# Kernel tuning notes

Hardware: AMD Instinct MI355X
Metric: run time of the kernel (lower is better)

The kernel has to match this reference:

```python
import jax, jax.numpy as jnp
import numpy as np

N_NODES = 100000
N_EDGES = 3200000
NUM_FEATURES = 5
HIDDEN = 64


def _gcn_layer(x, W, b, src, dst, norm, n_nodes):
    """One GCNConv: out = scatter_add(norm * (xW)[src] -> dst) + b.
    src/dst/norm already include self-loops and symmetric normalization."""
    h = x @ W                                  # [N, out_ch] small dense GEMM
    msg = h[src] * norm[:, None]               # [E+N, out_ch] gather + scale
    out = jax.ops.segment_sum(msg, dst, num_segments=n_nodes)
    return out + b


def _build_norm(edge_index, n_nodes):
    """Add self-loops, compute D^{-1/2}[src] * D^{-1/2}[dst] (GCN symmetric norm)."""
    loop = jnp.arange(n_nodes, dtype=edge_index.dtype)
    src = jnp.concatenate([edge_index[0], loop])
    dst = jnp.concatenate([edge_index[1], loop])
    deg = jax.ops.segment_sum(jnp.ones_like(dst, dtype=jnp.float32), dst,
                              num_segments=n_nodes)
    dis = jnp.where(deg > 0, jax.lax.rsqrt(deg), 0.0)  # deg^{-1/2}
    norm = dis[src] * dis[dst]
    return src, dst, norm


def setup_inputs() -> dict:
    key = jax.random.key(0)
    ks = jax.random.split(key, 8)
    x = jax.random.normal(ks[0], (N_NODES, NUM_FEATURES), dtype=jnp.float32)
    edge_index = jax.random.randint(ks[1], (2, N_EDGES), 0, N_NODES, dtype=jnp.int64)
    # glorot-ish scaled params
    W1 = jax.random.normal(ks[2], (NUM_FEATURES, HIDDEN), dtype=jnp.float32) * (1.0 / np.sqrt(NUM_FEATURES))
    b1 = jnp.zeros((HIDDEN,), dtype=jnp.float32)
    W2 = jax.random.normal(ks[3], (HIDDEN, HIDDEN), dtype=jnp.float32) * (1.0 / np.sqrt(HIDDEN))
    b2 = jnp.zeros((HIDDEN,), dtype=jnp.float32)
    W3 = jax.random.normal(ks[4], (HIDDEN, 1), dtype=jnp.float32) * (1.0 / np.sqrt(HIDDEN))
    b3 = jnp.zeros((1,), dtype=jnp.float32)
    return {"x": x, "edge_index": edge_index,
            "W1": W1, "b1": b1, "W2": W2, "b2": b2, "W3": W3, "b3": b3}


def reference(x, edge_index, W1, b1, W2, b2, W3, b3):
    n_nodes = x.shape[0]
    src, dst, norm = _build_norm(edge_index, n_nodes)
    h = jax.nn.relu(_gcn_layer(x, W1, b1, src, dst, norm, n_nodes))
    h = jax.nn.relu(_gcn_layer(h, W2, b2, src, dst, norm, n_nodes))
    out = _gcn_layer(h, W3, b3, src, dst, norm, n_nodes)  # [N, 1]
    return out
```

## Files before the change

kernel.cpp:

```cpp
#include <hip/hip_runtime.h>
#include <hip/hip_fp16.h>

#define NFEAT 5
#define HID 64
#define BSH 8
#define BNODES 256
#define NBK2 512
#define CHUNK 4096
#define ECAPMAX 12288

__global__ void k_binit(int* bcur, int ecap) {
    bcur[threadIdx.x] = threadIdx.x * ecap;
}

__global__ __launch_bounds__(256) void
k_bin(const int* __restrict__ src, const int* __restrict__ dst,
      int* bcur, unsigned* __restrict__ binned, int E) {
    __shared__ unsigned stg[CHUNK];
    __shared__ unsigned short bkt[CHUNK];
    __shared__ int hist[NBK2], base[NBK2], gb[NBK2];
    __shared__ int tmp[256];
    int t = threadIdx.x;
    int e0 = blockIdx.x * CHUNK;
    int cc = E - e0; if (cc > CHUNK) cc = CHUNK;
    hist[t] = 0; hist[t + 256] = 0;
    __syncthreads();
    unsigned me[16]; int mb[16]; unsigned short mr[16];
    const int4* src4 = (const int4*)(src + e0);
    const int4* dst4 = (const int4*)(dst + e0);
#pragma unroll
    for (int k = 0; k < 4; ++k) {
        int i4 = k * 256 + t;
        int ib = i4 * 4;
        int ss[4], dd[4];
        bool any = false;
        if (e0 + ib + 3 < E) {
            int4 s4 = src4[i4], d4 = dst4[i4];
            ss[0]=s4.x; ss[1]=s4.y; ss[2]=s4.z; ss[3]=s4.w;
            dd[0]=d4.x; dd[1]=d4.y; dd[2]=d4.z; dd[3]=d4.w;
            any = true;
#pragma unroll
            for (int j = 0; j < 4; ++j) mb[k*4+j] = 0;
        } else {
#pragma unroll
            for (int j = 0; j < 4; ++j) {
                if (e0 + ib + j < E) { ss[j]=src[e0+ib+j]; dd[j]=dst[e0+ib+j]; any=true; mb[k*4+j]=0; }
                else mb[k*4+j] = -1;
            }
        }
        if (any) {
#pragma unroll
            for (int j = 0; j < 4; ++j) {
                int idx = k * 4 + j;
                if (mb[idx] >= 0) {
                    mb[idx] = dd[j] >> BSH;
                    me[idx] = (unsigned)ss[j] | ((unsigned)(dd[j] & (BNODES - 1)) << 17);
                    mr[idx] = (unsigned short)atomicAdd(&hist[mb[idx]], 1);
                }
            }
        }
    }
    __syncthreads();
    int c0 = hist[2*t], c1 = hist[2*t + 1];
    int s = c0 + c1;
    tmp[t] = s;
    __syncthreads();
    for (int off = 1; off < 256; off <<= 1) {
        int a = (t >= off) ? tmp[t - off] : 0;
        __syncthreads();
        tmp[t] += a;
        __syncthreads();
    }
    int excl = tmp[t] - s;
    base[2*t]     = excl;
    base[2*t + 1] = excl + c0;
    gb[2*t]     = c0 ? atomicAdd(&bcur[2*t], c0) : 0;
    gb[2*t + 1] = c1 ? atomicAdd(&bcur[2*t + 1], c1) : 0;
    __syncthreads();
#pragma unroll
    for (int k = 0; k < 16; ++k)
        if (mb[k] >= 0) {
            int p = base[mb[k]] + mr[k];
            stg[p] = me[k];
            bkt[p] = (unsigned short)mb[k];
        }
    __syncthreads();
#pragma unroll
    for (int k = 0; k < 16; ++k) {
        int p = k * 256 + t;
        if (p < cc) {
            int b = bkt[p];
            binned[gb[b] + (p - base[b])] = stg[p];
        }
    }
}

__global__ __launch_bounds__(256) void
k_sort(const unsigned* __restrict__ binned, const int* __restrict__ bcur,
       const float* __restrict__ x, int* __restrict__ rpN, int* __restrict__ rpE,
       int* __restrict__ csr, float* __restrict__ dis, float* __restrict__ xs,
       int n, int ecap) {
    __shared__ unsigned short rank[ECAPMAX];
    __shared__ int hist[BNODES];
    __shared__ int cur[BNODES];
    __shared__ int tmp[256];
    int t = threadIdx.x, b = blockIdx.x;
    int e0 = b * ecap;
    int cnt = bcur[b] - e0;
    if (cnt > ecap) cnt = ecap;
    int v0 = b << BSH;
    int nv = n - v0; if (nv > BNODES) nv = BNODES;
    hist[t] = 0;
    __syncthreads();
    for (int i = t; i < cnt; i += 256) {
        int vl = binned[e0 + i] >> 17;
        rank[i] = (unsigned short)atomicAdd(&hist[vl], 1);
    }
    __syncthreads();
    if (t < nv) {
        int v = v0 + t;
        float dv = rsqrtf((float)hist[t] + 1.0f);
        dis[v] = dv;
        const float* xr = x + (size_t)v * NFEAT;
        float* xw = xs + (size_t)v * 8;
        xw[0] = dv * xr[0]; xw[1] = dv * xr[1]; xw[2] = dv * xr[2];
        xw[3] = dv * xr[3]; xw[4] = dv * xr[4];
        xw[5] = 0.f; xw[6] = 0.f; xw[7] = 0.f;
    }
    int c = hist[t];
    tmp[t] = c;
    __syncthreads();
    for (int off = 1; off < 256; off <<= 1) {
        int a = (t >= off) ? tmp[t - off] : 0;
        __syncthreads();
        tmp[t] += a;
        __syncthreads();
    }
    int excl = e0 + tmp[t] - c;
    cur[t] = excl;
    if (t < nv) { rpN[v0 + t] = excl; rpE[v0 + t] = excl + c; }
    __syncthreads();
    for (int i = t; i < cnt; i += 256) {
        unsigned e = binned[e0 + i];
        int vl = e >> 17;
        csr[cur[vl] + rank[i]] = (int)(e & 0x1FFFF);
    }
}

__global__ __launch_bounds__(256) void
k_layer1(const int* __restrict__ rpN, const int* __restrict__ rpE,
         const int* __restrict__ csr, const float* __restrict__ xs,
         const float* __restrict__ dis, const float* __restrict__ W1,
         const float* __restrict__ b1, __half* __restrict__ g1h, int n) {
    int wave = (blockIdx.x * blockDim.x + threadIdx.x) >> 6;
    int lane = threadIdx.x & 63;
    if (wave >= n) return;
    int v = wave;
    int r0 = rpN[v], r1 = rpE[v];
    float a0 = 0.f, a1 = 0.f, a2 = 0.f, a3 = 0.f, a4 = 0.f;
    for (int j = r0 + lane; j < r1; j += 64) {
        const float4* q = (const float4*)(xs + (size_t)csr[j] * 8);
        float4 qa = q[0], qb = q[1];
        a0 += qa.x; a1 += qa.y; a2 += qa.z; a3 += qa.w; a4 += qb.x;
    }
#pragma unroll
    for (int m = 32; m > 0; m >>= 1) {
        a0 += __shfl_xor(a0, m, 64); a1 += __shfl_xor(a1, m, 64);
        a2 += __shfl_xor(a2, m, 64); a3 += __shfl_xor(a3, m, 64);
        a4 += __shfl_xor(a4, m, 64);
    }
    float dv = dis[v];
    const float* pv = xs + (size_t)v * 8;
    a0 = dv * (a0 + pv[0]); a1 = dv * (a1 + pv[1]); a2 = dv * (a2 + pv[2]);
    a3 = dv * (a3 + pv[3]); a4 = dv * (a4 + pv[4]);
    int c = lane;
    float h = b1[c] + a0 * W1[c] + a1 * W1[64 + c] + a2 * W1[128 + c]
            + a3 * W1[192 + c] + a4 * W1[256 + c];
    g1h[(size_t)v * HID + c] = __float2half(dv * fmaxf(h, 0.0f));
}

__global__ __launch_bounds__(1024) void
k_layer23(const int* __restrict__ rpN, const int* __restrict__ rpE,
          const int* __restrict__ csr, const __half* __restrict__ g1h,
          const float* __restrict__ dis, const float* __restrict__ W2,
          const float* __restrict__ b2, const float* __restrict__ W3,
          float* __restrict__ svs, int n) {
    __shared__ float W2s[HID * HID];
    for (int i = threadIdx.x; i < HID * HID; i += 1024) W2s[i] = W2[i];
    __syncthreads();
    int wave = (blockIdx.x * blockDim.x + threadIdx.x) >> 6;
    int lane = threadIdx.x & 63;
    if (wave >= n) return;
    int v = wave;
    int r0 = rpN[v], r1 = rpE[v];
    float acc = __half2float(g1h[(size_t)v * HID + lane]);
    int j = r0;
    for (; j + 8 <= r1; j += 8) {
        int s0 = csr[j],     s1 = csr[j + 1], s2 = csr[j + 2], s3 = csr[j + 3];
        int s4 = csr[j + 4], s5 = csr[j + 5], s6 = csr[j + 6], s7 = csr[j + 7];
        float t0 = __half2float(g1h[(size_t)s0 * HID + lane]);
        float t1 = __half2float(g1h[(size_t)s1 * HID + lane]);
        float t2 = __half2float(g1h[(size_t)s2 * HID + lane]);
        float t3 = __half2float(g1h[(size_t)s3 * HID + lane]);
        float t4 = __half2float(g1h[(size_t)s4 * HID + lane]);
        float t5 = __half2float(g1h[(size_t)s5 * HID + lane]);
        float t6 = __half2float(g1h[(size_t)s6 * HID + lane]);
        float t7 = __half2float(g1h[(size_t)s7 * HID + lane]);
        acc += ((t0 + t1) + (t2 + t3)) + ((t4 + t5) + (t6 + t7));
    }
    for (; j < r1; ++j) acc += __half2float(g1h[(size_t)csr[j] * HID + lane]);
    float dv = dis[v];
    acc *= dv;
    float out = b2[lane];
#pragma unroll
    for (int k = 0; k < HID; ++k)
        out = fmaf(__shfl(acc, k, 64), W2s[(k << 6) + lane], out);
    out = fmaxf(out, 0.0f);
    float val = out * W3[lane];
#pragma unroll
    for (int m = 32; m > 0; m >>= 1) val += __shfl_xor(val, m, 64);
    if (lane == 0) svs[v] = dv * val;
}

__global__ __launch_bounds__(256) void
k_out(const int* __restrict__ rpN, const int* __restrict__ rpE,
      const int* __restrict__ csr, const float* __restrict__ svs,
      const float* __restrict__ dis, const float* __restrict__ b3,
      float* __restrict__ out, int n) {
    int wave = (blockIdx.x * blockDim.x + threadIdx.x) >> 6;
    int lane = threadIdx.x & 63;
    if (wave >= n) return;
    int v = wave;
    int r0 = rpN[v], r1 = rpE[v];
    float acc = (lane == 0) ? svs[v] : 0.f;
    for (int j = r0 + lane; j < r1; j += 64) acc += svs[csr[j]];
#pragma unroll
    for (int m = 32; m > 0; m >>= 1) acc += __shfl_xor(acc, m, 64);
    if (lane == 0) out[v] = b3[0] + dis[v] * acc;
}

extern "C" void kernel_launch(void* const* d_in, const int* in_sizes, int n_in,
                              void* d_out, int out_size, void* d_ws, size_t ws_size,
                              hipStream_t stream) {
    const float* x  = (const float*)d_in[0];
    const int*   ei = (const int*)d_in[1];
    const float* W1 = (const float*)d_in[2];
    const float* b1 = (const float*)d_in[3];
    const float* W2 = (const float*)d_in[4];
    const float* b2 = (const float*)d_in[5];
    const float* W3 = (const float*)d_in[6];
    const float* b3 = (const float*)d_in[7];
    float* out = (float*)d_out;

    const int n = out_size;
    const int E = in_sizes[1] / 2;
    const int* src = ei;
    const int* dst = ei + E;

    const int nbk = (n + BNODES - 1) / BNODES;
    int ecap = E / nbk;
    ecap += ecap / 8 + 1024;
    if (ecap > ECAPMAX) ecap = ECAPMAX;

    int*      bcur   = (int*)d_ws;
    int*      rpN    = bcur + 512;
    int*      rpE    = rpN + n;
    float*    dis    = (float*)(rpE + n);
    float*    svs    = dis + n;
    int*      csr    = (int*)(svs + n);
    unsigned* binned = (unsigned*)(csr + (size_t)nbk * ecap);
    float*    xs     = (float*)(binned + (size_t)nbk * ecap);
    __half*   g1h    = (__half*)binned;

    const int B = 256;
    const int nchunk = (E + CHUNK - 1) / CHUNK;
    const int gridW  = ((size_t)n * 64 + B - 1) / B;
    const int grid23 = ((size_t)n * 64 + 1023) / 1024;

    k_binit  <<<1, 512, 0, stream>>>(bcur, ecap);
    k_bin    <<<nchunk, 256, 0, stream>>>(src, dst, bcur, binned, E);
    k_sort   <<<nbk, 256, 0, stream>>>(binned, bcur, x, rpN, rpE, csr, dis, xs, n, ecap);
    k_layer1 <<<gridW, B, 0, stream>>>(rpN, rpE, csr, xs, dis, W1, b1, g1h, n);
    k_layer23<<<grid23, 1024, 0, stream>>>(rpN, rpE, csr, g1h, dis, W2, b2, W3, svs, n);
    k_out    <<<gridW, B, 0, stream>>>(rpN, rpE, csr, svs, dis, b3, out, n);
}
```

Measured before the change: 369.0 us.

## Sort neighbor lists and phase-sweep layer-2 gathers for cache locality

Layer 1 now uses a wave-wide bitonic sort to order each node's neighbor indices (for degree up to 64) and writes them back to the CSR. Layer 2/3 switches to a persistent grid where each wave owns 25 nodes and walks their sorted neighbor lists in phases over source-id ranges of 8192 nodes. This keeps gathered g1h rows inside a window small enough to stay in cache. The cost is per-wave register arrays (25 accumulators plus states), more serialized, lower-parallelism gather loops, and the extra sort and write-back in layer 1.

Result: slower. 796.0 us (+115.7%).

```diff
diff --git a/kernel.cpp b/kernel.cpp
--- a/kernel.cpp
+++ b/kernel.cpp
@@ -8,6 +8,12 @@
 #define NBK2 512
 #define CHUNK 4096
 #define ECAPMAX 12288
+
+#define L23_BLOCKS 1024
+#define L23_TPB 256
+#define L23_WAVES (L23_BLOCKS * L23_TPB / 64)
+#define NPW 25
+#define PHW 8192
 
 __global__ void k_binit(int* bcur, int ecap) {
     bcur[threadIdx.x] = threadIdx.x * ecap;
@@ -149,7 +155,7 @@
 
 __global__ __launch_bounds__(256) void
 k_layer1(const int* __restrict__ rpN, const int* __restrict__ rpE,
-         const int* __restrict__ csr, const float* __restrict__ xs,
+         int* __restrict__ csr, const float* __restrict__ xs,
          const float* __restrict__ dis, const float* __restrict__ W1,
          const float* __restrict__ b1, __half* __restrict__ g1h, int n) {
     int wave = (blockIdx.x * blockDim.x + threadIdx.x) >> 6;
@@ -157,11 +163,33 @@
     if (wave >= n) return;
     int v = wave;
     int r0 = rpN[v], r1 = rpE[v];
+    int cnt = r1 - r0;
     float a0 = 0.f, a1 = 0.f, a2 = 0.f, a3 = 0.f, a4 = 0.f;
-    for (int j = r0 + lane; j < r1; j += 64) {
-        const float4* q = (const float4*)(xs + (size_t)csr[j] * 8);
-        float4 qa = q[0], qb = q[1];
-        a0 += qa.x; a1 += qa.y; a2 += qa.z; a3 += qa.w; a4 += qb.x;
+    if (cnt <= 64) {
+        int key = (lane < cnt) ? csr[r0 + lane] : 0x7FFFFFFF;
+#pragma unroll
+        for (int k = 2; k <= 64; k <<= 1) {
+#pragma unroll
+            for (int j = k >> 1; j > 0; j >>= 1) {
+                int o = __shfl_xor(key, j, 64);
+                bool keepmin = (((lane & j) == 0) == ((lane & k) == 0));
+                int mn = key < o ? key : o;
+                int mx = key > o ? key : o;
+                key = keepmin ? mn : mx;
+            }
+        }
+        if (lane < cnt) {
+            csr[r0 + lane] = key;
+            const float4* q = (const float4*)(xs + (size_t)key * 8);
+            float4 qa = q[0], qb = q[1];
+            a0 = qa.x; a1 = qa.y; a2 = qa.z; a3 = qa.w; a4 = qb.x;
+        }
+    } else {
+        for (int j = r0 + lane; j < r1; j += 64) {
+            const float4* q = (const float4*)(xs + (size_t)csr[j] * 8);
+            float4 qa = q[0], qb = q[1];
+            a0 += qa.x; a1 += qa.y; a2 += qa.z; a3 += qa.w; a4 += qb.x;
+        }
     }
 #pragma unroll
     for (int m = 32; m > 0; m >>= 1) {
@@ -179,47 +207,93 @@
     g1h[(size_t)v * HID + c] = __float2half(dv * fmaxf(h, 0.0f));
 }
 
-__global__ __launch_bounds__(1024) void
+__global__ __launch_bounds__(L23_TPB, 4) void
 k_layer23(const int* __restrict__ rpN, const int* __restrict__ rpE,
           const int* __restrict__ csr, const __half* __restrict__ g1h,
           const float* __restrict__ dis, const float* __restrict__ W2,
           const float* __restrict__ b2, const float* __restrict__ W3,
           float* __restrict__ svs, int n) {
     __shared__ float W2s[HID * HID];
-    for (int i = threadIdx.x; i < HID * HID; i += 1024) W2s[i] = W2[i];
-    __syncthreads();
-    int wave = (blockIdx.x * blockDim.x + threadIdx.x) >> 6;
+    for (int i = threadIdx.x; i < HID * HID; i += L23_TPB) W2s[i] = W2[i];
+    __syncthreads();
+    int wv   = (blockIdx.x * L23_TPB + threadIdx.x) >> 6;
     int lane = threadIdx.x & 63;
-    if (wave >= n) return;
-    int v = wave;
-    int r0 = rpN[v], r1 = rpE[v];
-    float acc = __half2float(g1h[(size_t)v * HID + lane]);
-    int j = r0;
-    for (; j + 8 <= r1; j += 8) {
-        int s0 = csr[j],     s1 = csr[j + 1], s2 = csr[j + 2], s3 = csr[j + 3];
-        int s4 = csr[j + 4], s5 = csr[j + 5], s6 = csr[j + 6], s7 = csr[j + 7];
-        float t0 = __half2float(g1h[(size_t)s0 * HID + lane]);
-        float t1 = __half2float(g1h[(size_t)s1 * HID + lane]);
-        float t2 = __half2float(g1h[(size_t)s2 * HID + lane]);
-        float t3 = __half2float(g1h[(size_t)s3 * HID + lane]);
-        float t4 = __half2float(g1h[(size_t)s4 * HID + lane]);
-        float t5 = __half2float(g1h[(size_t)s5 * HID + lane]);
-        float t6 = __half2float(g1h[(size_t)s6 * HID + lane]);
-        float t7 = __half2float(g1h[(size_t)s7 * HID + lane]);
-        acc += ((t0 + t1) + (t2 + t3)) + ((t4 + t5) + (t6 + t7));
-    }
-    for (; j < r1; ++j) acc += __half2float(g1h[(size_t)csr[j] * HID + lane]);
-    float dv = dis[v];
-    acc *= dv;
-    float out = b2[lane];
-#pragma unroll
-    for (int k = 0; k < HID; ++k)
-        out = fmaf(__shfl(acc, k, 64), W2s[(k << 6) + lane], out);
-    out = fmaxf(out, 0.0f);
-    float val = out * W3[lane];
-#pragma unroll
-    for (int m = 32; m > 0; m >>= 1) val += __shfl_xor(val, m, 64);
-    if (lane == 0) svs[v] = dv * val;
+    int v0 = wv * NPW;
+
+    float    acc[NPW];
+    unsigned st[NPW];
+#pragma unroll
+    for (int i = 0; i < NPW; ++i) {
+        int v = v0 + i;
+        if (v < n) {
+            acc[i] = __half2float(g1h[((size_t)v << 6) + lane]);
+            int r0 = rpN[v], r1 = rpE[v];
+            int cnt = r1 - r0;
+            if (cnt > 255) {
+                for (int j = r0; j < r1; ++j)
+                    acc[i] += __half2float(g1h[((size_t)csr[j] << 6) + lane]);
+                st[i] = 0;
+            } else {
+                st[i] = ((unsigned)cnt << 24) | (unsigned)r0;
+            }
+        } else { acc[i] = 0.f; st[i] = 0; }
+    }
+
+    int nph = (n + PHW - 1) / PHW;
+    for (int ph = 0; ph < nph; ++ph) {
+        int bound = (ph + 1) * PHW;
+#pragma unroll
+        for (int i = 0; i < NPW; ++i) {
+            unsigned s_ = st[i];
+            if (s_ >= (1u << 24)) {
+                unsigned rem = s_ >> 24, p = s_ & 0xFFFFFFu;
+                while (rem) {
+                    int s = __builtin_amdgcn_readfirstlane(csr[p]);
+                    if (s >= bound) break;
+                    acc[i] += __half2float(g1h[((size_t)s << 6) + lane]);
+                    ++p; --rem;
+                }
+                st[i] = (rem << 24) | p;
+            }
+        }
+    }
+
+    for (int i = 0; i < NPW; ++i) {
+        int v = v0 + i;
+        if (v >= n) break;
+        float a = acc[0];
+#pragma unroll
+        for (int t = 1; t < NPW; ++t) if (i == t) a = acc[t];
+        float dv = dis[v];
+        a *= dv;
+        float outv = b2[lane];
+#pragma unroll
+        for (int k = 0; k < HID; ++k)
+            outv = fmaf(__shfl(a, k, 64), W2s[(k << 6) + lane], outv);
+        outv = fmaxf(outv, 0.0f);
+        float val = outv * W3[lane];
+#pragma unroll
+        for (int m = 32; m > 0; m >>= 1) val += __shfl_xor(val, m, 64);
+        if (lane == 0) svs[v] = dv * val;
+    }
+
+    for (int v = L23_WAVES * NPW + wv; v < n; v += L23_WAVES) {
+        int r0 = rpN[v], r1 = rpE[v];
+        float a = __half2float(g1h[((size_t)v << 6) + lane]);
+        for (int j = r0; j < r1; ++j)
+            a += __half2float(g1h[((size_t)csr[j] << 6) + lane]);
+        float dv = dis[v];
+        a *= dv;
+        float outv = b2[lane];
+#pragma unroll
+        for (int k = 0; k < HID; ++k)
+            outv = fmaf(__shfl(a, k, 64), W2s[(k << 6) + lane], outv);
+        outv = fmaxf(outv, 0.0f);
+        float val = outv * W3[lane];
+#pragma unroll
+        for (int m = 32; m > 0; m >>= 1) val += __shfl_xor(val, m, 64);
+        if (lane == 0) svs[v] = dv * val;
+    }
 }
 
 __global__ __launch_bounds__(256) void
@@ -275,12 +349,11 @@
     const int B = 256;
     const int nchunk = (E + CHUNK - 1) / CHUNK;
     const int gridW  = ((size_t)n * 64 + B - 1) / B;
-    const int grid23 = ((size_t)n * 64 + 1023) / 1024;
 
     k_binit  <<<1, 512, 0, stream>>>(bcur, ecap);
     k_bin    <<<nchunk, 256, 0, stream>>>(src, dst, bcur, binned, E);
     k_sort   <<<nbk, 256, 0, stream>>>(binned, bcur, x, rpN, rpE, csr, dis, xs, n, ecap);
     k_layer1 <<<gridW, B, 0, stream>>>(rpN, rpE, csr, xs, dis, W1, b1, g1h, n);
-    k_layer23<<<grid23, 1024, 0, stream>>>(rpN, rpE, csr, g1h, dis, W2, b2, W3, svs, n);
+    k_layer23<<<L23_BLOCKS, L23_TPB, 0, stream>>>(rpN, rpE, csr, g1h, dis, W2, b2, W3, svs, n);
     k_out    <<<gridW, B, 0, stream>>>(rpN, rpE, csr, svs, dis, b3, out, n);
 }
```
